# Optimization experiments

Measured on AMD Instinct MI355X. Metric: run time of the kernel, lower is better.

## Reference

```python
import jax, jax.numpy as jnp
import numpy as np
from jax import lax

WS = 8
HEADS = 8
QD = 64
VD = 256
B, H, W = 2, 256, 256
BN_EPS = 1e-5


def _rel_index(ws):
    coords = np.stack(np.meshgrid(np.arange(ws), np.arange(ws), indexing='ij'))  # (2, ws, ws)
    flat = coords.reshape(2, -1)                      # (2, ws*ws)
    rel = flat[:, :, None] - flat[:, None, :]         # (2, n, n)
    rel = rel.transpose(1, 2, 0).astype(np.int32)     # (n, n, 2)
    rel[..., 0] += ws - 1
    rel[..., 1] += ws - 1
    rel[..., 0] *= 2 * ws - 1
    return rel.sum(-1)                                # (n, n)


def setup_inputs() -> dict:
    key = jax.random.key(0)
    ks = jax.random.split(key, 8)
    inp = {
        'q': jax.random.normal(ks[0], (B, QD, H, W), jnp.float32),
        'v': jax.random.normal(ks[1], (B, VD, H, W), jnp.float32),
        'Wq': jax.random.normal(ks[2], (QD, QD), jnp.float32) * 0.05,
        'Wk': jax.random.normal(ks[3], (QD, QD), jnp.float32) * 0.05,
        'Wv': jax.random.normal(ks[4], (VD, VD), jnp.float32) * 0.05,
        'bias_table': jax.random.normal(ks[5], ((2 * WS - 1) ** 2, HEADS), jnp.float32) * 0.02,
        'dw_kernel': jax.random.normal(ks[6], (VD, 1, WS, WS), jnp.float32) * 0.05,
        'bn_gamma': jnp.ones((VD,), jnp.float32),
        'bn_beta': jnp.zeros((VD,), jnp.float32),
        'bn_mean': jnp.zeros((VD,), jnp.float32),
        'bn_var': jnp.ones((VD,), jnp.float32),
        'pw_kernel': jax.random.normal(ks[7], (VD, VD), jnp.float32) * 0.05,
        'rel_index': jnp.asarray(_rel_index(WS)),
    }
    return inp


def _window(x, heads, ws):
    # 'b (h d) (hh ws1) (ww ws2) -> (b hh ww) h (ws1 ws2) d'
    b, c, h, w = x.shape
    d = c // heads
    x = x.reshape(b, heads, d, h // ws, ws, w // ws, ws)
    x = x.transpose(0, 3, 5, 1, 4, 6, 2)  # b,hh,ww,h,ws1,ws2,d
    return x.reshape(b * (h // ws) * (w // ws), heads, ws * ws, d)


def _unwindow(x, b, heads, h, w, ws):
    # '(b hh ww) h (ws1 ws2) d -> b (h d) (hh ws1) (ww ws2)'
    d = x.shape[-1]
    x = x.reshape(b, h // ws, w // ws, heads, ws, ws, d)
    x = x.transpose(0, 3, 6, 1, 4, 2, 5)  # b,h,d,hh,ws1,ww,ws2
    return x.reshape(b, heads * d, h, w)


def reference(q, v, Wq, Wk, Wv, bias_table, dw_kernel, bn_gamma, bn_beta,
              bn_mean, bn_var, pw_kernel, rel_index):
    b, c, h, w = v.shape  # H,W divisible by WS -> pad() is a no-op
    scale = (QD // HEADS) ** -0.5

    # 1x1 conv projections (Mode='conv': q=self.q(q), k=self.k(q))
    qp = jnp.einsum('bchw,oc->bohw', q, Wq)
    kp = jnp.einsum('bchw,oc->bohw', qp, Wk)
    vp = jnp.einsum('bchw,oc->bohw', v, Wv)

    qw = _window(qp, HEADS, WS)
    kw = _window(kp, HEADS, WS)
    vw = _window(vp, HEADS, WS)

    dots = jnp.einsum('bhnd,bhmd->bhnm', qw, kw) * scale
    n = WS * WS
    bias = bias_table[rel_index.reshape(-1)].reshape(n, n, HEADS).transpose(2, 0, 1)
    attn = jax.nn.softmax(dots + bias[None], axis=-1)
    out = jnp.einsum('bhnm,bhmd->bhnd', attn, vw)

    out = _unwindow(out, b, HEADS, h, w, WS)  # (b, C, H, W); crop [:H,:W] is no-op

    # pad_out: reflect pad right/bottom by 1
    out = jnp.pad(out, ((0, 0), (0, 0), (0, 1), (0, 1)), mode='reflect')

    # proj = SeparableConvBN(kernel=WS): depthwise conv -> BN(eval) -> 1x1 conv
    pad = (WS - 1) // 2
    out = lax.conv_general_dilated(out, dw_kernel, (1, 1), ((pad, pad), (pad, pad)),
                                   feature_group_count=c,
                                   dimension_numbers=('NCHW', 'OIHW', 'NCHW'))
    inv = bn_gamma / jnp.sqrt(bn_var + BN_EPS)
    out = out * inv[None, :, None, None] + (bn_beta - bn_mean * inv)[None, :, None, None]
    out = jnp.einsum('bchw,oc->bohw', out, pw_kernel)
    return out[:, :, :h, :w]
```

## Files before the change

### kernel.cpp

```cpp
#include <hip/hip_runtime.h>
#include <cstddef>

#define HWN 65536
#define SCALE 0.35355339059327373f

typedef __bf16 bf16x8_t __attribute__((ext_vector_type(8)));
typedef float  f32x4_t  __attribute__((ext_vector_type(4)));

static __device__ __forceinline__ ushort f2bf(float f) {
    uint u = __float_as_uint(f);
    u = u + 0x7fffu + ((u >> 16) & 1u);
    return (ushort)(u >> 16);
}
static __device__ __forceinline__ float bf2f(ushort b) {
    return __uint_as_float(((uint)b) << 16);
}

__global__ __launch_bounds__(256) void bias_pre(
    const float* __restrict__ bt, const int* __restrict__ ri,
    float* __restrict__ biasF)
{
    int g = blockIdx.x * 256 + threadIdx.x;
    int h    = g >> 12;
    int rem  = g & 4095;
    int tile = rem >> 8;
    int lane = (rem >> 2) & 63;
    int r    = rem & 3;
    int i = tile >> 2, j = tile & 3;
    int qd = lane >> 4, ln = lane & 15;
    int m = i * 16 + qd * 4 + r;
    int n = j * 16 + ln;
    biasF[g] = bt[ri[n * 64 + m] * 8 + h];
}

__global__ __launch_bounds__(256) void conv1x1_64(
    const float* __restrict__ X, const float* __restrict__ W,
    float* __restrict__ Y)
{
    int gp = blockIdx.x * 256 + threadIdx.x;
    int b  = gp >> 16;
    int p  = gp & 65535;
    const float* Xb = X + (size_t)b * 64 * HWN + p;
    float* Yb       = Y + (size_t)b * 64 * HWN + p;

    float xr[64];
#pragma unroll
    for (int c = 0; c < 64; c++) xr[c] = Xb[(size_t)c * HWN];

#pragma unroll 4
    for (int o = 0; o < 64; o++) {
        const float* Wr = W + o * 64;
        float acc = 0.f;
#pragma unroll
        for (int c = 0; c < 64; c++) acc = fmaf(Wr[c], xr[c], acc);
        Yb[(size_t)o * HWN] = acc;
    }
}

template <typename XT, typename YT>
__global__ __launch_bounds__(256) void gemm256(
    const XT* __restrict__ X, const float* __restrict__ W, YT* __restrict__ Y)
{
    __shared__ ushort Al[128 * 72];
    __shared__ ushort Bl[128 * 72];

    int b   = blockIdx.z;
    int oB  = blockIdx.y * 128;
    int pB  = blockIdx.x * 128;
    int tid = threadIdx.x;

    const XT* Xb = X + (size_t)b * 256 * HWN;
    YT*       Yb = Y + (size_t)b * 256 * HWN;

    int wv = tid >> 6, lane = tid & 63;
    int wm = (wv >> 1) * 64, wn = (wv & 1) * 64;
    int qd = lane >> 4, ln = lane & 15;

    int kgB = tid >> 4;
    int pgB = tid & 15;
    int p0  = pgB * 8;

    f32x4_t acc[4][4];
#pragma unroll
    for (int i = 0; i < 4; i++)
#pragma unroll
        for (int j = 0; j < 4; j++) acc[i][j] = {0.f, 0.f, 0.f, 0.f};

    for (int kc = 0; kc < 256; kc += 64) {
#pragma unroll
        for (int s = 0; s < 4; s++) {
            int u = tid + s * 256;
            int m = u >> 3, kg = u & 7;
            const float4* src = (const float4*)&W[(oB + m) * 256 + kc + kg * 8];
            float4 w0 = src[0], w1 = src[1];
            uint4 pk;
            pk.x = f2bf(w0.x) | ((uint)f2bf(w0.y) << 16);
            pk.y = f2bf(w0.z) | ((uint)f2bf(w0.w) << 16);
            pk.z = f2bf(w1.x) | ((uint)f2bf(w1.y) << 16);
            pk.w = f2bf(w1.z) | ((uint)f2bf(w1.w) << 16);
            *(uint4*)&Al[m * 72 + kg * 8] = pk;
        }
        ushort r[4][8];
#pragma unroll
        for (int i = 0; i < 4; i++) {
            int c = kc + kgB * 4 + i;
            if constexpr (sizeof(XT) == 4) {
                const float4* s = (const float4*)&Xb[(size_t)c * HWN + pB + p0];
                float4 x0 = s[0], x1 = s[1];
                r[i][0] = f2bf(x0.x); r[i][1] = f2bf(x0.y);
                r[i][2] = f2bf(x0.z); r[i][3] = f2bf(x0.w);
                r[i][4] = f2bf(x1.x); r[i][5] = f2bf(x1.y);
                r[i][6] = f2bf(x1.z); r[i][7] = f2bf(x1.w);
            } else {
                uint4 u = *(const uint4*)&Xb[(size_t)c * HWN + pB + p0];
                r[i][0] = u.x & 0xffff; r[i][1] = u.x >> 16;
                r[i][2] = u.y & 0xffff; r[i][3] = u.y >> 16;
                r[i][4] = u.z & 0xffff; r[i][5] = u.z >> 16;
                r[i][6] = u.w & 0xffff; r[i][7] = u.w >> 16;
            }
        }
        {
            int g   = kgB >> 1;
            int sub = (kgB & 1) * 4;
#pragma unroll
            for (int j = 0; j < 8; j++) {
                int n = p0 + j;
                ushort4 col = make_ushort4(r[0][j], r[1][j], r[2][j], r[3][j]);
                *(ushort4*)&Bl[n * 72 + ((g ^ (pgB & 7)) << 3) + sub] = col;
            }
        }
        __syncthreads();

#pragma unroll
        for (int ks = 0; ks < 2; ks++) {
            bf16x8_t af[4], bf[4];
#pragma unroll
            for (int i = 0; i < 4; i++)
                af[i] = *(const bf16x8_t*)&Al[(wm + i * 16 + ln) * 72 + ks * 32 + qd * 8];
#pragma unroll
            for (int j = 0; j < 4; j++) {
                int n = wn + j * 16 + ln;
                int g = ks * 4 + qd;
                bf[j] = *(const bf16x8_t*)&Bl[n * 72 + ((g ^ ((n >> 3) & 7)) << 3)];
            }
#pragma unroll
            for (int i = 0; i < 4; i++)
#pragma unroll
                for (int j = 0; j < 4; j++)
                    acc[i][j] = __builtin_amdgcn_mfma_f32_16x16x32_bf16(
                        af[i], bf[j], acc[i][j], 0, 0, 0);
        }
        __syncthreads();
    }

#pragma unroll
    for (int i = 0; i < 4; i++) {
#pragma unroll
        for (int j = 0; j < 4; j++) {
#pragma unroll
            for (int rr = 0; rr < 4; rr++) {
                int o = oB + wm + i * 16 + qd * 4 + rr;
                int p = pB + wn + j * 16 + ln;
                if constexpr (sizeof(YT) == 4)
                    Yb[(size_t)o * HWN + p] = acc[i][j][rr];
                else
                    Yb[(size_t)o * HWN + p] = f2bf(acc[i][j][rr]);
            }
        }
    }
}

__global__ __launch_bounds__(64, 4) void win_attn(
    const float* __restrict__ QP, const float* __restrict__ KP,
    const ushort* VP, ushort* OUT, const float* __restrict__ biasF)
{
    __shared__ char smem[10240];
    ushort* ql = (ushort*)smem;
    ushort* kq = (ushort*)(smem + 5120);
    ushort* pl = (ushort*)smem;
    float*  ol = (float*)smem;

    int bx   = blockIdx.x;
    int head = bx & 7;
    int win  = bx >> 3;
    int wc   = win & 31;
    int wr   = (win >> 5) & 31;
    int b    = win >> 10;

    int n   = threadIdx.x;
    int ws1 = n >> 3, ws2 = n & 7;
    int pos = (wr * 8 + ws1) * 256 + wc * 8 + ws2;

    const float*  qb = QP + ((size_t)(b * 64 + head * 8)) * HWN + pos;
    const float*  kb = KP + ((size_t)(b * 64 + head * 8)) * HWN + pos;
    const ushort* vbase = VP + ((size_t)(b * 256 + head * 32)) * HWN
                             + (size_t)(wr * 8) * 256 + wc * 8;
    ushort*       ob = OUT + ((size_t)(b * 256 + head * 32)) * HWN + pos;

    uint qh[4], qlw[4], kh[4], klw[4];
#pragma unroll
    for (int d = 0; d < 4; d++) {
        float q0 = qb[(size_t)(2 * d)     * HWN] * SCALE;
        float q1 = qb[(size_t)(2 * d + 1) * HWN] * SCALE;
        ushort qh0 = f2bf(q0), qh1 = f2bf(q1);
        ushort ql0 = f2bf(q0 - bf2f(qh0)), ql1 = f2bf(q1 - bf2f(qh1));
        qh[d]  = (uint)qh0 | ((uint)qh1 << 16);
        qlw[d] = (uint)ql0 | ((uint)ql1 << 16);
        float k0 = kb[(size_t)(2 * d)     * HWN];
        float k1 = kb[(size_t)(2 * d + 1) * HWN];
        ushort kh0 = f2bf(k0), kh1 = f2bf(k1);
        ushort kl0 = f2bf(k0 - bf2f(kh0)), kl1 = f2bf(k1 - bf2f(kh1));
        kh[d]  = (uint)kh0 | ((uint)kh1 << 16);
        klw[d] = (uint)kl0 | ((uint)kl1 << 16);
    }
    uint4 z4 = make_uint4(0u, 0u, 0u, 0u);
    uint4 qhv = make_uint4(qh[0], qh[1], qh[2], qh[3]);
    uint4 qlv = make_uint4(qlw[0], qlw[1], qlw[2], qlw[3]);
    uint4 khv = make_uint4(kh[0], kh[1], kh[2], kh[3]);
    uint4 klv = make_uint4(klw[0], klw[1], klw[2], klw[3]);
    *(uint4*)&ql[n * 40 +  0] = qhv;
    *(uint4*)&ql[n * 40 +  8] = qlv;
    *(uint4*)&ql[n * 40 + 16] = qhv;
    *(uint4*)&ql[n * 40 + 24] = z4;
    *(uint4*)&kq[n * 40 +  0] = khv;
    *(uint4*)&kq[n * 40 +  8] = khv;
    *(uint4*)&kq[n * 40 + 16] = klv;
    *(uint4*)&kq[n * 40 + 24] = z4;
    __syncthreads();

    int ln = n & 15, qd = n >> 4;

    f32x4_t sacc[4][4];
    const float* bfr = biasF + (size_t)head * 4096;
#pragma unroll
    for (int i = 0; i < 4; i++)
#pragma unroll
        for (int j = 0; j < 4; j++)
            sacc[i][j] = *(const f32x4_t*)&bfr[((i * 4 + j) * 64 + n) * 4];

    bf16x8_t kf[4];
#pragma unroll
    for (int i = 0; i < 4; i++)
        kf[i] = *(const bf16x8_t*)&kq[(16 * i + ln) * 40 + qd * 8];
#pragma unroll
    for (int j = 0; j < 4; j++) {
        bf16x8_t qf = *(const bf16x8_t*)&ql[(16 * j + ln) * 40 + qd * 8];
#pragma unroll
        for (int i = 0; i < 4; i++)
            sacc[i][j] = __builtin_amdgcn_mfma_f32_16x16x32_bf16(
                kf[i], qf, sacc[i][j], 0, 0, 0);
    }

    float rs[4];
#pragma unroll
    for (int j = 0; j < 4; j++) {
        float m0 = sacc[0][j][0];
#pragma unroll
        for (int i = 0; i < 4; i++)
#pragma unroll
            for (int r = 0; r < 4; r++) m0 = fmaxf(m0, sacc[i][j][r]);
        m0 = fmaxf(m0, __shfl_xor(m0, 16));
        m0 = fmaxf(m0, __shfl_xor(m0, 32));
        float s0 = 0.f;
#pragma unroll
        for (int i = 0; i < 4; i++)
#pragma unroll
            for (int r = 0; r < 4; r++) {
                float e = __expf(sacc[i][j][r] - m0);
                sacc[i][j][r] = e;
                s0 += e;
            }
        s0 += __shfl_xor(s0, 16);
        s0 += __shfl_xor(s0, 32);
        rs[j] = 1.f / s0;
    }

    __syncthreads();

#pragma unroll
    for (int i = 0; i < 4; i++)
#pragma unroll
        for (int j = 0; j < 4; j++) {
            uint lo = (uint)f2bf(sacc[i][j][0] * rs[j])
                    | ((uint)f2bf(sacc[i][j][1] * rs[j]) << 16);
            uint hi = (uint)f2bf(sacc[i][j][2] * rs[j])
                    | ((uint)f2bf(sacc[i][j][3] * rs[j]) << 16);
            *(uint2*)&pl[(16 * j + ln) * 72 + 16 * i + qd * 4] = make_uint2(lo, hi);
        }
    __syncthreads();

    f32x4_t acc[4][2];
#pragma unroll
    for (int i = 0; i < 4; i++)
#pragma unroll
        for (int j = 0; j < 2; j++) acc[i][j] = {0.f, 0.f, 0.f, 0.f};

#pragma unroll
    for (int kc = 0; kc < 2; kc++) {
        bf16x8_t af[4], bfv[2];
#pragma unroll
        for (int i = 0; i < 4; i++)
            af[i] = *(const bf16x8_t*)&pl[(16 * i + ln) * 72 + kc * 32 + qd * 8];
#pragma unroll
        for (int j = 0; j < 2; j++) {
            const ushort* vp8 = vbase + (size_t)(16 * j + ln) * HWN
                                      + (kc * 4 + qd) * 256;
            uint4 u = *(const uint4*)vp8;
            bfv[j] = *(const bf16x8_t*)&u;
        }
#pragma unroll
        for (int i = 0; i < 4; i++)
#pragma unroll
            for (int j = 0; j < 2; j++)
                acc[i][j] = __builtin_amdgcn_mfma_f32_16x16x32_bf16(
                    af[i], bfv[j], acc[i][j], 0, 0, 0);
    }
    __syncthreads();

#pragma unroll
    for (int i = 0; i < 4; i++)
#pragma unroll
        for (int j = 0; j < 2; j++)
#pragma unroll
            for (int r = 0; r < 4; r++)
                ol[(16 * i + qd * 4 + r) * 36 + j * 16 + ln] = acc[i][j][r];
    __syncthreads();

#pragma unroll
    for (int c = 0; c < 8; c++) {
        float4 o4 = *(const float4*)&ol[n * 36 + c * 4];
        ob[(size_t)(c * 4 + 0) * HWN] = f2bf(o4.x);
        ob[(size_t)(c * 4 + 1) * HWN] = f2bf(o4.y);
        ob[(size_t)(c * 4 + 2) * HWN] = f2bf(o4.z);
        ob[(size_t)(c * 4 + 3) * HWN] = f2bf(o4.w);
    }
}

__global__ __launch_bounds__(256, 5) void dwconv_bn(
    const ushort* __restrict__ A, const float* __restrict__ DW,
    const float* __restrict__ gamma, const float* __restrict__ beta,
    const float* __restrict__ mean, const float* __restrict__ var,
    ushort* __restrict__ O)
{
    __shared__ ushort til[39 * 272];

    int c  = blockIdx.y;
    int b  = blockIdx.z;
    int tY = blockIdx.x * 32;
    int tid = threadIdx.x;

    const ushort* Ab = A + ((size_t)(b * 256 + c)) * HWN;

    for (int li = tid; li < 39 * 34; li += 256) {
        int yr = li / 34;
        int ck = li - yr * 34;
        int iy = tY - 3 + yr;
        uint4 u = make_uint4(0u, 0u, 0u, 0u);
        if (iy >= 0 && iy <= 256) {
            int sy = (iy == 256) ? 254 : iy;
            const ushort* row = Ab + sy * 256;
            if (ck >= 1 && ck <= 32) {
                u = *(const uint4*)&row[ck * 8 - 8];
            } else if (ck == 33) {
                u.x = (uint)row[254];
            }
        }
        *(uint4*)&til[yr * 272 + ck * 8] = u;
    }

    float w[64];
#pragma unroll
    for (int i = 0; i < 16; i++)
        *(float4*)&w[i * 4] = *(const float4*)&DW[c * 64 + i * 4];

    __syncthreads();

    float inv = gamma[c] * rsqrtf(var[c] + 1e-5f);
    float add = fmaf(-mean[c], inv, beta[c]);

    int xg = tid & 31;
    int yg = tid >> 5;
    int xo = xg * 8;
    int yb = yg * 4;

    float acc[4][8];
#pragma unroll
    for (int j = 0; j < 4; j++)
#pragma unroll
        for (int p = 0; p < 8; p++) acc[j][p] = 0.f;

#pragma unroll
    for (int r = 0; r < 11; r++) {
        const uint4* rp = (const uint4*)&til[(yb + r) * 272 + xo];
        uint4 a0 = rp[0], a1 = rp[1], a2 = rp[2];
        uint u[12] = {a0.x, a0.y, a0.z, a0.w,
                      a1.x, a1.y, a1.z, a1.w,
                      a2.x, a2.y, a2.z, a2.w};
        float vals[16];
#pragma unroll
        for (int t = 2; t < 10; t++) {
            vals[2 * (t - 2)]     = __uint_as_float(u[t] << 16);
            vals[2 * (t - 2) + 1] = __uint_as_float(u[t] & 0xffff0000u);
        }
        int jlo = (r - 7 < 0) ? 0 : r - 7;
        int jhi = (r < 3) ? r : 3;
#pragma unroll
        for (int j = jlo; j <= jhi; j++) {
            const float* wr = &w[(r - j) * 8];
#pragma unroll
            for (int kx = 0; kx < 8; kx++) {
                float wt = wr[kx];
#pragma unroll
                for (int p = 0; p < 8; p++)
                    acc[j][p] = fmaf(vals[1 + p + kx], wt, acc[j][p]);
            }
        }
    }

    ushort* Ob = O + ((size_t)(b * 256 + c)) * HWN + (tY + yb) * 256 + xo;
#pragma unroll
    for (int j = 0; j < 4; j++) {
        uint4 st;
        st.x = (uint)f2bf(fmaf(acc[j][0], inv, add))
             | ((uint)f2bf(fmaf(acc[j][1], inv, add)) << 16);
        st.y = (uint)f2bf(fmaf(acc[j][2], inv, add))
             | ((uint)f2bf(fmaf(acc[j][3], inv, add)) << 16);
        st.z = (uint)f2bf(fmaf(acc[j][4], inv, add))
             | ((uint)f2bf(fmaf(acc[j][5], inv, add)) << 16);
        st.w = (uint)f2bf(fmaf(acc[j][6], inv, add))
             | ((uint)f2bf(fmaf(acc[j][7], inv, add)) << 16);
        *(uint4*)&Ob[j * 256] = st;
    }
}

extern "C" void kernel_launch(void* const* d_in, const int* in_sizes, int n_in,
                              void* d_out, int out_size, void* d_ws, size_t ws_size,
                              hipStream_t stream)
{
    (void)in_sizes; (void)n_in; (void)ws_size;

    const float* q    = (const float*)d_in[0];
    const float* v    = (const float*)d_in[1];
    const float* Wq   = (const float*)d_in[2];
    const float* Wk   = (const float*)d_in[3];
    const float* Wv   = (const float*)d_in[4];
    const float* bt   = (const float*)d_in[5];
    const float* dw   = (const float*)d_in[6];
    const float* gam  = (const float*)d_in[7];
    const float* bet  = (const float*)d_in[8];
    const float* mean = (const float*)d_in[9];
    const float* var  = (const float*)d_in[10];
    const float* pw   = (const float*)d_in[11];
    const int*   ri   = (const int*)d_in[12];
    float* out = (float*)d_out;

    float*  qp  = (float*)d_ws;
    float*  kp  = qp + (size_t)2 * 64 * HWN;
    ushort* vp  = (ushort*)(kp + (size_t)2 * 64 * HWN);
    ushort* ao  = vp;
    ushort* dwo = vp + (size_t)2 * 256 * HWN;
    float*  biasF = out + (size_t)out_size - 32768;

    bias_pre<<<128, 256, 0, stream>>>(bt, ri, biasF);
    conv1x1_64<<<512, 256, 0, stream>>>(q, Wq, qp);
    conv1x1_64<<<512, 256, 0, stream>>>(qp, Wk, kp);
    gemm256<float, ushort><<<dim3(512, 2, 2), 256, 0, stream>>>(v, Wv, vp);
    win_attn<<<16384, 64, 0, stream>>>(qp, kp, vp, ao, biasF);
    dwconv_bn<<<dim3(8, 256, 2), 256, 0, stream>>>(ao, dw, gam, bet, mean, var, dwo);
    gemm256<ushort, float><<<dim3(512, 2, 2), 256, 0, stream>>>(dwo, pw, out);
}
```

Measured before the change: 618.6 us.

## Prefetch GEMM tiles into registers, pre-pack weights to bf16, fuse Q/K projections

The 256-channel GEMM now loads the next K-chunk of weights and activations into registers while the current chunk runs MFMA, giving software-pipelined global loads. Weights are converted to bf16 once by a small pack kernel, so the GEMM no longer converts them per tile. The two 64-channel projections are fused into one kernel that keeps the Q result in registers to compute K, removing one full read of qp. In exchange, register pressure rises in both the GEMM and the fused conv, and the packed weights live in scratch space reused from out and qp, which depends on the later kernels not having overwritten those buffers yet.

```diff
diff --git a/kernel.cpp b/kernel.cpp
--- a/kernel.cpp
+++ b/kernel.cpp
@@ -33,33 +33,56 @@
     biasF[g] = bt[ri[n * 64 + m] * 8 + h];
 }
 
-__global__ __launch_bounds__(256) void conv1x1_64(
-    const float* __restrict__ X, const float* __restrict__ W,
-    float* __restrict__ Y)
+__global__ __launch_bounds__(256) void pack_w(
+    const float* __restrict__ Wf, ushort* __restrict__ Wb)
+{
+    int g = blockIdx.x * 256 + threadIdx.x;
+    float4 v = *(const float4*)&Wf[g * 4];
+    ushort4 o = make_ushort4(f2bf(v.x), f2bf(v.y), f2bf(v.z), f2bf(v.w));
+    *(ushort4*)&Wb[g * 4] = o;
+}
+
+__global__ __launch_bounds__(256) void conv1x1_qk(
+    const float* __restrict__ X, const float* __restrict__ WQ,
+    const float* __restrict__ WK, float* __restrict__ QP,
+    float* __restrict__ KP)
 {
     int gp = blockIdx.x * 256 + threadIdx.x;
     int b  = gp >> 16;
     int p  = gp & 65535;
     const float* Xb = X + (size_t)b * 64 * HWN + p;
-    float* Yb       = Y + (size_t)b * 64 * HWN + p;
+    float* Qb = QP + (size_t)b * 64 * HWN + p;
+    float* Kb = KP + (size_t)b * 64 * HWN + p;
 
     float xr[64];
 #pragma unroll
     for (int c = 0; c < 64; c++) xr[c] = Xb[(size_t)c * HWN];
 
+    float qr[64];
 #pragma unroll 4
     for (int o = 0; o < 64; o++) {
-        const float* Wr = W + o * 64;
+        const float* Wr = WQ + o * 64;
         float acc = 0.f;
 #pragma unroll
         for (int c = 0; c < 64; c++) acc = fmaf(Wr[c], xr[c], acc);
-        Yb[(size_t)o * HWN] = acc;
+        qr[o] = acc;
+        Qb[(size_t)o * HWN] = acc;
+    }
+
+#pragma unroll 4
+    for (int o = 0; o < 64; o++) {
+        const float* Wr = WK + o * 64;
+        float acc = 0.f;
+#pragma unroll
+        for (int c = 0; c < 64; c++) acc = fmaf(Wr[c], qr[c], acc);
+        Kb[(size_t)o * HWN] = acc;
     }
 }
 
 template <typename XT, typename YT>
 __global__ __launch_bounds__(256) void gemm256(
-    const XT* __restrict__ X, const float* __restrict__ W, YT* __restrict__ Y)
+    const XT* __restrict__ X, const ushort* __restrict__ Wb,
+    YT* __restrict__ Y)
 {
     __shared__ ushort Al[128 * 72];
     __shared__ ushort Bl[128 * 72];
@@ -86,33 +109,45 @@
 #pragma unroll
         for (int j = 0; j < 4; j++) acc[i][j] = {0.f, 0.f, 0.f, 0.f};
 
-    for (int kc = 0; kc < 256; kc += 64) {
+    uint4  aw[4];
+    uint4  xw[4];
+    float4 xf[4][2];
+
+#pragma unroll
+    for (int s = 0; s < 4; s++) {
+        int u = tid + s * 256;
+        int m = u >> 3, kg = u & 7;
+        aw[s] = *(const uint4*)&Wb[(size_t)(oB + m) * 256 + kg * 8];
+    }
+#pragma unroll
+    for (int i = 0; i < 4; i++) {
+        int c = kgB * 4 + i;
+        if constexpr (sizeof(XT) == 4) {
+            const float4* s = (const float4*)&Xb[(size_t)c * HWN + pB + p0];
+            xf[i][0] = s[0]; xf[i][1] = s[1];
+        } else {
+            xw[i] = *(const uint4*)&Xb[(size_t)c * HWN + pB + p0];
+        }
+    }
+
+    for (int kt = 0; kt < 4; kt++) {
 #pragma unroll
         for (int s = 0; s < 4; s++) {
             int u = tid + s * 256;
             int m = u >> 3, kg = u & 7;
-            const float4* src = (const float4*)&W[(oB + m) * 256 + kc + kg * 8];
-            float4 w0 = src[0], w1 = src[1];
-            uint4 pk;
-            pk.x = f2bf(w0.x) | ((uint)f2bf(w0.y) << 16);
-            pk.y = f2bf(w0.z) | ((uint)f2bf(w0.w) << 16);
-            pk.z = f2bf(w1.x) | ((uint)f2bf(w1.y) << 16);
-            pk.w = f2bf(w1.z) | ((uint)f2bf(w1.w) << 16);
-            *(uint4*)&Al[m * 72 + kg * 8] = pk;
+            *(uint4*)&Al[m * 72 + kg * 8] = aw[s];
         }
         ushort r[4][8];
 #pragma unroll
         for (int i = 0; i < 4; i++) {
-            int c = kc + kgB * 4 + i;
             if constexpr (sizeof(XT) == 4) {
-                const float4* s = (const float4*)&Xb[(size_t)c * HWN + pB + p0];
-                float4 x0 = s[0], x1 = s[1];
+                float4 x0 = xf[i][0], x1 = xf[i][1];
                 r[i][0] = f2bf(x0.x); r[i][1] = f2bf(x0.y);
                 r[i][2] = f2bf(x0.z); r[i][3] = f2bf(x0.w);
                 r[i][4] = f2bf(x1.x); r[i][5] = f2bf(x1.y);
                 r[i][6] = f2bf(x1.z); r[i][7] = f2bf(x1.w);
             } else {
-                uint4 u = *(const uint4*)&Xb[(size_t)c * HWN + pB + p0];
+                uint4 u = xw[i];
                 r[i][0] = u.x & 0xffff; r[i][1] = u.x >> 16;
                 r[i][2] = u.y & 0xffff; r[i][3] = u.y >> 16;
                 r[i][4] = u.z & 0xffff; r[i][5] = u.z >> 16;
@@ -130,6 +165,26 @@
             }
         }
         __syncthreads();
+
+        if (kt < 3) {
+            int kc = (kt + 1) * 64;
+#pragma unroll
+            for (int s = 0; s < 4; s++) {
+                int u = tid + s * 256;
+                int m = u >> 3, kg = u & 7;
+                aw[s] = *(const uint4*)&Wb[(size_t)(oB + m) * 256 + kc + kg * 8];
+            }
+#pragma unroll
+            for (int i = 0; i < 4; i++) {
+                int c = kc + kgB * 4 + i;
+                if constexpr (sizeof(XT) == 4) {
+                    const float4* s = (const float4*)&Xb[(size_t)c * HWN + pB + p0];
+                    xf[i][0] = s[0]; xf[i][1] = s[1];
+                } else {
+                    xw[i] = *(const uint4*)&Xb[(size_t)c * HWN + pB + p0];
+                }
+            }
+        }
 
 #pragma unroll
         for (int ks = 0; ks < 2; ks++) {
@@ -460,12 +515,15 @@
     ushort* ao  = vp;
     ushort* dwo = vp + (size_t)2 * 256 * HWN;
     float*  biasF = out + (size_t)out_size - 32768;
+    ushort* wvb = (ushort*)out;
+    ushort* pwb = (ushort*)qp;
 
     bias_pre<<<128, 256, 0, stream>>>(bt, ri, biasF);
-    conv1x1_64<<<512, 256, 0, stream>>>(q, Wq, qp);
-    conv1x1_64<<<512, 256, 0, stream>>>(qp, Wk, kp);
-    gemm256<float, ushort><<<dim3(512, 2, 2), 256, 0, stream>>>(v, Wv, vp);
+    pack_w<<<64, 256, 0, stream>>>(Wv, wvb);
+    conv1x1_qk<<<512, 256, 0, stream>>>(q, Wq, Wk, qp, kp);
+    gemm256<float, ushort><<<dim3(512, 2, 2), 256, 0, stream>>>(v, wvb, vp);
     win_attn<<<16384, 64, 0, stream>>>(qp, kp, vp, ao, biasF);
+    pack_w<<<64, 256, 0, stream>>>(pw, pwb);
     dwconv_bn<<<dim3(8, 256, 2), 256, 0, stream>>>(ao, dw, gam, bet, mean, var, dwo);
-    gemm256<ushort, float><<<dim3(512, 2, 2), 256, 0, stream>>>(dwo, pw, out);
-}
+    gemm256<ushort, float><<<dim3(512, 2, 2), 256, 0, stream>>>(dwo, pwb, out);
+}
```

After: 654.9 us. 1.06x slower.

## Fuse Q and K 1x1 projections into one MFMA kernel with split-bf16

Applied to the files above, without the earlier changes.

Replaces the two scalar FP32 conv1x1_64 launches with one kernel that computes both the Q and K projections on bf16 MFMA. Near-fp32 accuracy comes from a three-term hi/lo bf16 split. The intermediate qp stays in shared memory, re-split, and feeds the K projection directly, which saves a launch and a global round-trip of qp. The cost is extra conversion work and shared-memory pressure, along with a small accuracy change from dropping the lo*lo term.

```diff
diff --git a/kernel.cpp b/kernel.cpp
--- a/kernel.cpp
+++ b/kernel.cpp
@@ -33,27 +33,178 @@
     biasF[g] = bt[ri[n * 64 + m] * 8 + h];
 }
 
-__global__ __launch_bounds__(256) void conv1x1_64(
-    const float* __restrict__ X, const float* __restrict__ W,
-    float* __restrict__ Y)
+__global__ __launch_bounds__(256) void qk_mfma(
+    const float* __restrict__ X, const float* __restrict__ WQ,
+    const float* __restrict__ WK, float* __restrict__ QP,
+    float* __restrict__ KP)
 {
-    int gp = blockIdx.x * 256 + threadIdx.x;
-    int b  = gp >> 16;
-    int p  = gp & 65535;
-    const float* Xb = X + (size_t)b * 64 * HWN + p;
-    float* Yb       = Y + (size_t)b * 64 * HWN + p;
-
-    float xr[64];
-#pragma unroll
-    for (int c = 0; c < 64; c++) xr[c] = Xb[(size_t)c * HWN];
-
-#pragma unroll 4
-    for (int o = 0; o < 64; o++) {
-        const float* Wr = W + o * 64;
-        float acc = 0.f;
-#pragma unroll
-        for (int c = 0; c < 64; c++) acc = fmaf(Wr[c], xr[c], acc);
-        Yb[(size_t)o * HWN] = acc;
+    __shared__ ushort Bh[128 * 72];
+    __shared__ ushort Blo[128 * 72];
+    __shared__ ushort Wh[2][64 * 72];
+    __shared__ ushort Wl[2][64 * 72];
+
+    int b   = blockIdx.y;
+    int pB  = blockIdx.x * 128;
+    int tid = threadIdx.x;
+
+    const float* Xb = X + (size_t)b * 64 * HWN;
+    float* Qb = QP + (size_t)b * 64 * HWN;
+    float* Kb = KP + (size_t)b * 64 * HWN;
+
+    int wv = tid >> 6, lane = tid & 63;
+    int wn = wv * 32;
+    int qd = lane >> 4, ln = lane & 15;
+
+    int kgB = tid >> 4;
+    int pgB = tid & 15;
+    int p0  = pgB * 8;
+
+#pragma unroll
+    for (int mat = 0; mat < 2; mat++) {
+        const float* Wsrc = mat ? WK : WQ;
+#pragma unroll
+        for (int s = 0; s < 2; s++) {
+            int u = tid + s * 256;
+            int m = u >> 3, kg = u & 7;
+            const float4* src = (const float4*)&Wsrc[m * 64 + kg * 8];
+            float4 w0 = src[0], w1 = src[1];
+            float wf[8] = {w0.x, w0.y, w0.z, w0.w, w1.x, w1.y, w1.z, w1.w};
+            uint4 ph, pl;
+            uint* php = (uint*)&ph; uint* plp = (uint*)&pl;
+#pragma unroll
+            for (int e = 0; e < 4; e++) {
+                ushort h0 = f2bf(wf[2*e]),   h1 = f2bf(wf[2*e+1]);
+                ushort l0 = f2bf(wf[2*e]   - bf2f(h0));
+                ushort l1 = f2bf(wf[2*e+1] - bf2f(h1));
+                php[e] = (uint)h0 | ((uint)h1 << 16);
+                plp[e] = (uint)l0 | ((uint)l1 << 16);
+            }
+            *(uint4*)&Wh[mat][m * 72 + kg * 8] = ph;
+            *(uint4*)&Wl[mat][m * 72 + kg * 8] = pl;
+        }
+    }
+
+    {
+        ushort rh[4][8], rl[4][8];
+#pragma unroll
+        for (int i = 0; i < 4; i++) {
+            int c = kgB * 4 + i;
+            const float4* s = (const float4*)&Xb[(size_t)c * HWN + pB + p0];
+            float4 x0 = s[0], x1 = s[1];
+            float xv[8] = {x0.x, x0.y, x0.z, x0.w, x1.x, x1.y, x1.z, x1.w};
+#pragma unroll
+            for (int e = 0; e < 8; e++) {
+                ushort h = f2bf(xv[e]);
+                rh[i][e] = h;
+                rl[i][e] = f2bf(xv[e] - bf2f(h));
+            }
+        }
+        int g   = kgB >> 1;
+        int sub = (kgB & 1) * 4;
+#pragma unroll
+        for (int j = 0; j < 8; j++) {
+            int n = p0 + j;
+            int off = n * 72 + ((g ^ (pgB & 7)) << 3) + sub;
+            *(ushort4*)&Bh[off]  = make_ushort4(rh[0][j], rh[1][j], rh[2][j], rh[3][j]);
+            *(ushort4*)&Blo[off] = make_ushort4(rl[0][j], rl[1][j], rl[2][j], rl[3][j]);
+        }
+    }
+    __syncthreads();
+
+    f32x4_t acc1[4][2];
+#pragma unroll
+    for (int i = 0; i < 4; i++)
+#pragma unroll
+        for (int j = 0; j < 2; j++) acc1[i][j] = {0.f, 0.f, 0.f, 0.f};
+
+#pragma unroll
+    for (int t = 0; t < 3; t++) {
+        const ushort* A = (t == 2) ? Wl[0] : Wh[0];
+        const ushort* B = (t == 1) ? Blo   : Bh;
+#pragma unroll
+        for (int ks = 0; ks < 2; ks++) {
+            bf16x8_t af[4];
+#pragma unroll
+            for (int i = 0; i < 4; i++)
+                af[i] = *(const bf16x8_t*)&A[(i * 16 + ln) * 72 + ks * 32 + qd * 8];
+#pragma unroll
+            for (int j = 0; j < 2; j++) {
+                int n = wn + j * 16 + ln;
+                bf16x8_t bfj = *(const bf16x8_t*)
+                    &B[n * 72 + (((ks * 4 + qd) ^ ((n >> 3) & 7)) << 3)];
+#pragma unroll
+                for (int i = 0; i < 4; i++)
+                    acc1[i][j] = __builtin_amdgcn_mfma_f32_16x16x32_bf16(
+                        af[i], bfj, acc1[i][j], 0, 0, 0);
+            }
+        }
+    }
+    __syncthreads();
+
+#pragma unroll
+    for (int i = 0; i < 4; i++) {
+        int g   = i * 2 + (qd >> 1);
+        int sub = (qd & 1) * 4;
+#pragma unroll
+        for (int j = 0; j < 2; j++) {
+            int n = wn + j * 16 + ln;
+            int off = n * 72 + ((g ^ ((n >> 3) & 7)) << 3) + sub;
+            ushort h[4], l[4];
+#pragma unroll
+            for (int r = 0; r < 4; r++) {
+                float v = acc1[i][j][r];
+                h[r] = f2bf(v);
+                l[r] = f2bf(v - bf2f(h[r]));
+            }
+            *(uint2*)&Bh[off]  = make_uint2((uint)h[0] | ((uint)h[1] << 16),
+                                            (uint)h[2] | ((uint)h[3] << 16));
+            *(uint2*)&Blo[off] = make_uint2((uint)l[0] | ((uint)l[1] << 16),
+                                            (uint)l[2] | ((uint)l[3] << 16));
+        }
+    }
+    __syncthreads();
+
+    f32x4_t acc2[4][2];
+#pragma unroll
+    for (int i = 0; i < 4; i++)
+#pragma unroll
+        for (int j = 0; j < 2; j++) acc2[i][j] = {0.f, 0.f, 0.f, 0.f};
+
+#pragma unroll
+    for (int t = 0; t < 3; t++) {
+        const ushort* A = (t == 2) ? Wl[1] : Wh[1];
+        const ushort* B = (t == 1) ? Blo   : Bh;
+#pragma unroll
+        for (int ks = 0; ks < 2; ks++) {
+            bf16x8_t af[4];
+#pragma unroll
+            for (int i = 0; i < 4; i++)
+                af[i] = *(const bf16x8_t*)&A[(i * 16 + ln) * 72 + ks * 32 + qd * 8];
+#pragma unroll
+            for (int j = 0; j < 2; j++) {
+                int n = wn + j * 16 + ln;
+                bf16x8_t bfj = *(const bf16x8_t*)
+                    &B[n * 72 + (((ks * 4 + qd) ^ ((n >> 3) & 7)) << 3)];
+#pragma unroll
+                for (int i = 0; i < 4; i++)
+                    acc2[i][j] = __builtin_amdgcn_mfma_f32_16x16x32_bf16(
+                        af[i], bfj, acc2[i][j], 0, 0, 0);
+            }
+        }
+    }
+
+#pragma unroll
+    for (int i = 0; i < 4; i++) {
+#pragma unroll
+        for (int j = 0; j < 2; j++) {
+            int p = pB + wn + j * 16 + ln;
+#pragma unroll
+            for (int r = 0; r < 4; r++) {
+                int o = i * 16 + qd * 4 + r;
+                Qb[(size_t)o * HWN + p] = acc1[i][j][r];
+                Kb[(size_t)o * HWN + p] = acc2[i][j][r];
+            }
+        }
     }
 }
 
@@ -462,8 +613,7 @@
     float*  biasF = out + (size_t)out_size - 32768;
 
     bias_pre<<<128, 256, 0, stream>>>(bt, ri, biasF);
-    conv1x1_64<<<512, 256, 0, stream>>>(q, Wq, qp);
-    conv1x1_64<<<512, 256, 0, stream>>>(qp, Wk, kp);
+    qk_mfma<<<dim3(512, 2), 256, 0, stream>>>(q, Wq, Wk, qp, kp);
     gemm256<float, ushort><<<dim3(512, 2, 2), 256, 0, stream>>>(v, Wv, vp);
     win_attn<<<16384, 64, 0, stream>>>(qp, kp, vp, ao, biasF);
     dwconv_bn<<<dim3(8, 256, 2), 256, 0, stream>>>(ao, dw, gam, bet, mean, var, dwo);
```

Measured after the change: 494.9 us. 1.25x faster.
